# Kernel tuning notes

Hardware: AMD Instinct MI355X
Metric: run time of the kernel (lower is better)

## Reference

```python
import jax, jax.numpy as jnp
import numpy as np

N_NODES = 100000
N_EDGES = 1600000


def gcn_layer(x, src, dst, W, b, n_nodes):
    # PyG GCNConv: h = x @ W; add self-loops; sym-normalized scatter-add; + bias
    h = x @ W
    loop = jnp.arange(n_nodes, dtype=src.dtype)
    si = jnp.concatenate([src, loop])
    di = jnp.concatenate([dst, loop])
    deg = jax.ops.segment_sum(jnp.ones(si.shape[0], h.dtype), di, num_segments=n_nodes)
    dinv = jax.lax.rsqrt(deg)  # deg >= 1 due to self-loops
    norm = dinv[si] * dinv[di]              # [E+N]
    msgs = h[si] * norm[:, None]            # gather-scale
    out = jax.ops.segment_sum(msgs, di, num_segments=n_nodes)  # scatter-add
    return out + b


def setup_inputs() -> dict:
    key = jax.random.key(0)
    ks = jax.random.split(key, 8)
    x = jax.random.normal(ks[0], (N_NODES, 8), dtype=jnp.float32)
    edge_index = jax.random.randint(ks[1], (2, N_EDGES), 0, N_NODES, dtype=jnp.int32)
    W1 = jax.random.normal(ks[2], (8, 32), dtype=jnp.float32) * 0.3
    b1 = jax.random.normal(ks[3], (32,), dtype=jnp.float32) * 0.1
    W2 = jax.random.normal(ks[4], (32, 16), dtype=jnp.float32) * 0.2
    b2 = jax.random.normal(ks[5], (16,), dtype=jnp.float32) * 0.1
    Wfc = jax.random.normal(ks[6], (16, 1), dtype=jnp.float32) * 0.25
    bfc = jax.random.normal(ks[7], (1,), dtype=jnp.float32) * 0.1
    return {"x": x, "edge_index": edge_index, "W1": W1, "b1": b1,
            "W2": W2, "b2": b2, "Wfc": Wfc, "bfc": bfc}


def reference(x, edge_index, W1, b1, W2, b2, Wfc, bfc):
    n = x.shape[0]
    src, dst = edge_index[0], edge_index[1]
    h = jax.nn.relu(gcn_layer(x, src, dst, W1, b1, n))
    h = jax.nn.relu(gcn_layer(h, src, dst, W2, b2, n))
    return jax.nn.sigmoid(h @ Wfc + bfc)  # [N, 1]
```

## Files before the change

kernel.cpp:

```cpp
#include <hip/hip_runtime.h>
#include <math.h>

#define N_NODES 100000
#define N_EDGES 1600000

#define NB_SHIFT 7
#define NB 128
#define NBINS 782
#define RCAP 2432
#define BCHUNK 2048
#define BINBLOCKS ((N_EDGES + BCHUNK - 1) / BCHUNK)
#define LCAP 8
#define SPB 16

__device__ __forceinline__ unsigned int pack_bf2(float a, float b) {
    unsigned int ua = __float_as_uint(a), ub = __float_as_uint(b);
    ua += 0x7FFFu + ((ua >> 16) & 1u);
    ub += 0x7FFFu + ((ub >> 16) & 1u);
    return (ua >> 16) | (ub & 0xFFFF0000u);
}
__device__ __forceinline__ float bf_lo(unsigned int u) { return __uint_as_float(u << 16); }
__device__ __forceinline__ float bf_hi(unsigned int u) { return __uint_as_float(u & 0xFFFF0000u); }

#define QR(v) { v += __shfl_xor(v, 1, 64); v += __shfl_xor(v, 2, 64); }

__global__ __launch_bounds__(512) void k_bin(const int* __restrict__ src, const int* __restrict__ dst,
                                             unsigned char* __restrict__ cnt_tab, int* __restrict__ log,
                                             int* __restrict__ spill_rec, int* __restrict__ spill_bin, int e) {
    __shared__ int lcnt[NBINS];
    __shared__ int lbuf[NBINS * LCAP];
    __shared__ int sp_rec[SPB];
    __shared__ int sp_bin[SPB];
    __shared__ int sp_n;
    int tid = threadIdx.x, blk = blockIdx.x;
    for (int b = tid; b < NBINS; b += 512) lcnt[b] = 0;
    if (tid == 0) sp_n = 0;
    __syncthreads();
    int base = blk * BCHUNK;
    int end = min(base + BCHUNK, e);
    int i0 = base + tid * 4;
    if (i0 + 4 <= end) {
        int4 s4 = *(const int4*)(src + i0);
        int4 d4 = *(const int4*)(dst + i0);
        int ss[4] = { s4.x, s4.y, s4.z, s4.w };
        int dd[4] = { d4.x, d4.y, d4.z, d4.w };
#pragma unroll
        for (int k = 0; k < 4; ++k) {
            int d = dd[k], s = ss[k];
            int b = d >> NB_SHIFT;
            int rec = (s << NB_SHIFT) | (d & (NB - 1));
            int slot = atomicAdd(&lcnt[b], 1);
            if (slot < LCAP) {
                lbuf[b * LCAP + slot] = rec;
            } else {
                int kk = atomicAdd(&sp_n, 1);
                if (kk < SPB) { sp_rec[kk] = rec; sp_bin[kk] = b; }
            }
        }
    } else {
        for (int i = i0; i < end; ++i) {
            int d = dst[i], s = src[i];
            int b = d >> NB_SHIFT;
            int rec = (s << NB_SHIFT) | (d & (NB - 1));
            int slot = atomicAdd(&lcnt[b], 1);
            if (slot < LCAP) {
                lbuf[b * LCAP + slot] = rec;
            } else {
                int kk = atomicAdd(&sp_n, 1);
                if (kk < SPB) { sp_rec[kk] = rec; sp_bin[kk] = b; }
            }
        }
    }
    __syncthreads();
    int* lrow = log + blk * NBINS * LCAP;
    for (int b = tid; b < NBINS; b += 512) {
        int c = min(lcnt[b], LCAP);
        cnt_tab[blk * NBINS + b] = (unsigned char)c;
        if (c > 0) *(int4*)(lrow + b * LCAP)     = *(const int4*)&lbuf[b * LCAP];
        if (c > 4) *(int4*)(lrow + b * LCAP + 4) = *(const int4*)&lbuf[b * LCAP + 4];
    }
    if (tid < SPB) {
        int valid = tid < min(sp_n, SPB);
        spill_rec[blk * SPB + tid] = valid ? sp_rec[tid] : 0;
        spill_bin[blk * SPB + tid] = valid ? sp_bin[tid] : -1;
    }
}

__global__ __launch_bounds__(512) void k_sort(const unsigned char* __restrict__ cnt_tab, const int* __restrict__ log,
                                              const int* __restrict__ spill_rec, const int* __restrict__ spill_bin,
                                              int* __restrict__ gcur, int* __restrict__ regions,
                                              const float* __restrict__ x, float* __restrict__ dinv,
                                              unsigned int* __restrict__ gxu, int* __restrict__ row_start) {
    __shared__ int ccnt[BINBLOCKS];
    __shared__ int coff[BINBLOCKS];
    __shared__ int wtot[8];
    __shared__ int msum_s;
    __shared__ int sp_take;
    __shared__ int lrec[RCAP];
    __shared__ int lsort[RCAP];
    __shared__ int cnt[NB];
    __shared__ int stt[NB];
    __shared__ int cur[NB];
    __shared__ float di_s[NB];
    int b = blockIdx.x, tid = threadIdx.x;
    int lane = tid & 63, wv = tid >> 6;

    for (int c = tid; c < BINBLOCKS; c += 512) ccnt[c] = cnt_tab[c * NBINS + b];
    if (tid == 0) sp_take = 0;
    if (tid < NB) cnt[tid] = 0;
    __syncthreads();
    {
        int c0 = tid * 2, c1 = c0 + 1;
        int v0 = (c0 < BINBLOCKS) ? ccnt[c0] : 0;
        int v1 = (c1 < BINBLOCKS) ? ccnt[c1] : 0;
        int v = v0 + v1, sc = v;
#pragma unroll
        for (int off = 1; off < 64; off <<= 1) {
            int t = __shfl_up(sc, off, 64);
            if (lane >= off) sc += t;
        }
        if (lane == 63) wtot[wv] = sc;
        __syncthreads();
        if (tid == 0) {
            int acc = 0;
#pragma unroll
            for (int w = 0; w < 8; ++w) { int t = wtot[w]; wtot[w] = acc; acc += t; }
            msum_s = acc;
        }
        __syncthreads();
        int basep = sc - v + wtot[wv];
        if (c0 < BINBLOCKS) coff[c0] = basep;
        if (c1 < BINBLOCKS) coff[c1] = basep + v0;
    }
    __syncthreads();
    for (int c = tid; c < BINBLOCKS; c += 512) {
        int cc = ccnt[c];
        if (cc > 0) {
            const int* chunk = log + (c * NBINS + b) * LCAP;
            int p = coff[c];
            int4 v0 = *(const int4*)chunk;
            int r;
            r = v0.x; if (p < RCAP)              { lrec[p] = r;     atomicAdd(&cnt[r & (NB - 1)], 1); }
            r = v0.y; if (cc > 1 && p + 1 < RCAP){ lrec[p + 1] = r; atomicAdd(&cnt[r & (NB - 1)], 1); }
            r = v0.z; if (cc > 2 && p + 2 < RCAP){ lrec[p + 2] = r; atomicAdd(&cnt[r & (NB - 1)], 1); }
            r = v0.w; if (cc > 3 && p + 3 < RCAP){ lrec[p + 3] = r; atomicAdd(&cnt[r & (NB - 1)], 1); }
            if (cc > 4) {
                int4 v1 = *(const int4*)(chunk + 4);
                r = v1.x; if (p + 4 < RCAP)          { lrec[p + 4] = r; atomicAdd(&cnt[r & (NB - 1)], 1); }
                r = v1.y; if (cc > 5 && p + 5 < RCAP){ lrec[p + 5] = r; atomicAdd(&cnt[r & (NB - 1)], 1); }
                r = v1.z; if (cc > 6 && p + 6 < RCAP){ lrec[p + 6] = r; atomicAdd(&cnt[r & (NB - 1)], 1); }
                r = v1.w; if (cc > 7 && p + 7 < RCAP){ lrec[p + 7] = r; atomicAdd(&cnt[r & (NB - 1)], 1); }
            }
        }
    }
    for (int jj = tid; jj < BINBLOCKS * SPB; jj += 512) {
        if (spill_bin[jj] == b) {
            int p = atomicAdd(&sp_take, 1);
            int pos = msum_s + p;
            if (pos < RCAP) {
                int rec = spill_rec[jj];
                lrec[pos] = rec;
                atomicAdd(&cnt[rec & (NB - 1)], 1);
            }
        }
    }
    __syncthreads();
    int m = min(msum_s + sp_take, RCAP);
    if (tid == 0) gcur[b] = m;
    if (tid < 64) {
        int c0 = cnt[lane], c1 = cnt[64 + lane];
        int s0 = c0, s1 = c1;
#pragma unroll
        for (int off = 1; off < 64; off <<= 1) {
            int t0 = __shfl_up(s0, off, 64);
            int t1 = __shfl_up(s1, off, 64);
            if (lane >= off) { s0 += t0; s1 += t1; }
        }
        s1 += __shfl(s0, 63, 64);
        stt[lane] = s0 - c0;
        stt[64 + lane] = s1 - c1;
    }
    __syncthreads();
    int node0 = b << NB_SHIFT;
    if (tid < NB) {
        cur[tid] = stt[tid];
        float d = rsqrtf((float)cnt[tid] + 1.0f);
        di_s[tid] = d;
        row_start[b * NB + tid] = b * RCAP + stt[tid];
        int node = node0 + tid;
        if (node < N_NODES) dinv[node] = d;
    }
    __syncthreads();
    {
        int l = tid >> 2, p = tid & 3;
        int node = node0 + l;
        if (node < N_NODES) {
            const float2* x2 = (const float2*)x;
            float2 xv = x2[node * 4 + p];
            float d = di_s[l];
            gxu[node * 4 + p] = pack_bf2(xv.x * d, xv.y * d);
        }
    }
    for (int j = tid; j < m; j += 512) {
        int rec = lrec[j];
        int pos = atomicAdd(&cur[rec & (NB - 1)], 1);
        lsort[pos] = rec >> NB_SHIFT;
    }
    __syncthreads();
    int* wb = regions + b * RCAP;
    for (int j = tid; j < m; j += 512) wb[j] = lsort[j];
}

__global__ __launch_bounds__(512) void k_agg1_mlp(const int* __restrict__ gcur, const int* __restrict__ regions,
                                                  const int* __restrict__ row_start,
                                                  const unsigned int* __restrict__ gxu,
                                                  const float* __restrict__ dinv,
                                                  const float* __restrict__ W1, const float* __restrict__ b1,
                                                  const float* __restrict__ W2,
                                                  unsigned int* __restrict__ g2u) {
    __shared__ int lsort[RCAP];
    __shared__ float wsh[800];
    int b = blockIdx.x, tid = threadIdx.x;
    int m = gcur[b];
    const int* rrow = regions + b * RCAP;
    for (int j = tid; j < m; j += 512) lsort[j] = rrow[j];
    for (int i2 = tid; i2 < 800; i2 += 512)
        wsh[i2] = (i2 < 256) ? W1[i2] : (i2 < 288) ? b1[i2 - 256] : W2[i2 - 288];
    __syncthreads();
    int l = tid >> 2, q = tid & 3;
    int node = (b << NB_SHIFT) + l;
    if (node >= N_NODES) return;
    int js = row_start[node] - b * RCAP;
    int je = (l < NB - 1) ? (row_start[node + 1] - b * RCAP) : m;
    const uint4* gx4 = (const uint4*)gxu;
    float a0 = 0.f, a1 = 0.f, a2 = 0.f, a3 = 0.f, a4 = 0.f, a5 = 0.f, a6 = 0.f, a7 = 0.f;
    if (q == 0) {
        uint4 u = gx4[node];
        a0 = bf_lo(u.x); a1 = bf_hi(u.x); a2 = bf_lo(u.y); a3 = bf_hi(u.y);
        a4 = bf_lo(u.z); a5 = bf_hi(u.z); a6 = bf_lo(u.w); a7 = bf_hi(u.w);
    }
    int j = js + q;
    for (; j + 4 < je; j += 8) {
        int s0 = lsort[j], s1 = lsort[j + 4];
        uint4 u = gx4[s0];
        uint4 w = gx4[s1];
        a0 += bf_lo(u.x); a1 += bf_hi(u.x); a2 += bf_lo(u.y); a3 += bf_hi(u.y);
        a4 += bf_lo(u.z); a5 += bf_hi(u.z); a6 += bf_lo(u.w); a7 += bf_hi(u.w);
        a0 += bf_lo(w.x); a1 += bf_hi(w.x); a2 += bf_lo(w.y); a3 += bf_hi(w.y);
        a4 += bf_lo(w.z); a5 += bf_hi(w.z); a6 += bf_lo(w.w); a7 += bf_hi(w.w);
    }
    if (j < je) {
        uint4 u = gx4[lsort[j]];
        a0 += bf_lo(u.x); a1 += bf_hi(u.x); a2 += bf_lo(u.y); a3 += bf_hi(u.y);
        a4 += bf_lo(u.z); a5 += bf_hi(u.z); a6 += bf_lo(u.w); a7 += bf_hi(u.w);
    }
    QR(a0); QR(a1); QR(a2); QR(a3); QR(a4); QR(a5); QR(a6); QR(a7);
    float di = dinv[node];
    float y[8] = { a0 * di, a1 * di, a2 * di, a3 * di, a4 * di, a5 * di, a6 * di, a7 * di };
    const float* W1s = wsh;
    const float* b1s = wsh + 256;
    const float* W2s = wsh + 288;
    float hh[8];
#pragma unroll
    for (int ff = 0; ff < 8; ++ff) {
        int f = q * 8 + ff;
        float sa = b1s[f];
#pragma unroll
        for (int k = 0; k < 8; ++k) sa = fmaf(y[k], W1s[k * 32 + f], sa);
        hh[ff] = fmaxf(0.f, sa);
    }
    float g[16];
#pragma unroll
    for (int o = 0; o < 16; ++o) {
        float sa = 0.f;
#pragma unroll
        for (int ff = 0; ff < 8; ++ff) sa = fmaf(hh[ff], W2s[(q * 8 + ff) * 16 + o], sa);
        g[o] = sa;
    }
#pragma unroll
    for (int o = 0; o < 16; ++o) QR(g[o]);
    int f0 = q * 4;
    uint2 pk = make_uint2(pack_bf2(g[f0] * di, g[f0 + 1] * di),
                          pack_bf2(g[f0 + 2] * di, g[f0 + 3] * di));
    ((uint2*)g2u)[node * 4 + q] = pk;
}

__global__ __launch_bounds__(512) void k_agg2_final(const int* __restrict__ gcur, const int* __restrict__ regions,
                                                    const int* __restrict__ row_start,
                                                    const unsigned int* __restrict__ g2u,
                                                    const float* __restrict__ dinv,
                                                    const float* __restrict__ b2, const float* __restrict__ Wfc,
                                                    const float* __restrict__ bfc, float* __restrict__ out) {
    __shared__ int lsort[RCAP];
    int b = blockIdx.x, tid = threadIdx.x;
    int m = gcur[b];
    const int* rrow = regions + b * RCAP;
    for (int j = tid; j < m; j += 512) lsort[j] = rrow[j];
    __syncthreads();
    int l = tid >> 2, q = tid & 3;
    int node = (b << NB_SHIFT) + l;
    if (node >= N_NODES) return;
    int js = row_start[node] - b * RCAP;
    int je = (l < NB - 1) ? (row_start[node + 1] - b * RCAP) : m;
    const uint4* g24 = (const uint4*)g2u;
    float a[16];
#pragma unroll
    for (int f = 0; f < 16; ++f) a[f] = 0.f;
    if (q == 0) {
        uint4 u0 = g24[node * 2], u1 = g24[node * 2 + 1];
        a[0] = bf_lo(u0.x); a[1] = bf_hi(u0.x); a[2] = bf_lo(u0.y); a[3] = bf_hi(u0.y);
        a[4] = bf_lo(u0.z); a[5] = bf_hi(u0.z); a[6] = bf_lo(u0.w); a[7] = bf_hi(u0.w);
        a[8] = bf_lo(u1.x); a[9] = bf_hi(u1.x); a[10] = bf_lo(u1.y); a[11] = bf_hi(u1.y);
        a[12] = bf_lo(u1.z); a[13] = bf_hi(u1.z); a[14] = bf_lo(u1.w); a[15] = bf_hi(u1.w);
    }
    int j = js + q;
    for (; j + 4 < je; j += 8) {
        int s0 = lsort[j], s1 = lsort[j + 4];
        uint4 u0 = g24[s0 * 2], u1 = g24[s0 * 2 + 1];
        uint4 w0 = g24[s1 * 2], w1 = g24[s1 * 2 + 1];
        a[0] += bf_lo(u0.x); a[1] += bf_hi(u0.x); a[2] += bf_lo(u0.y); a[3] += bf_hi(u0.y);
        a[4] += bf_lo(u0.z); a[5] += bf_hi(u0.z); a[6] += bf_lo(u0.w); a[7] += bf_hi(u0.w);
        a[8] += bf_lo(u1.x); a[9] += bf_hi(u1.x); a[10] += bf_lo(u1.y); a[11] += bf_hi(u1.y);
        a[12] += bf_lo(u1.z); a[13] += bf_hi(u1.z); a[14] += bf_lo(u1.w); a[15] += bf_hi(u1.w);
        a[0] += bf_lo(w0.x); a[1] += bf_hi(w0.x); a[2] += bf_lo(w0.y); a[3] += bf_hi(w0.y);
        a[4] += bf_lo(w0.z); a[5] += bf_hi(w0.z); a[6] += bf_lo(w0.w); a[7] += bf_hi(w0.w);
        a[8] += bf_lo(w1.x); a[9] += bf_hi(w1.x); a[10] += bf_lo(w1.y); a[11] += bf_hi(w1.y);
        a[12] += bf_lo(w1.z); a[13] += bf_hi(w1.z); a[14] += bf_lo(w1.w); a[15] += bf_hi(w1.w);
    }
    if (j < je) {
        int s0 = lsort[j];
        uint4 u0 = g24[s0 * 2], u1 = g24[s0 * 2 + 1];
        a[0] += bf_lo(u0.x); a[1] += bf_hi(u0.x); a[2] += bf_lo(u0.y); a[3] += bf_hi(u0.y);
        a[4] += bf_lo(u0.z); a[5] += bf_hi(u0.z); a[6] += bf_lo(u0.w); a[7] += bf_hi(u0.w);
        a[8] += bf_lo(u1.x); a[9] += bf_hi(u1.x); a[10] += bf_lo(u1.y); a[11] += bf_hi(u1.y);
        a[12] += bf_lo(u1.z); a[13] += bf_hi(u1.z); a[14] += bf_lo(u1.w); a[15] += bf_hi(u1.w);
    }
#pragma unroll
    for (int f = 0; f < 16; ++f) QR(a[f]);
    if (q == 0) {
        float di = dinv[node];
        float z = bfc[0];
#pragma unroll
        for (int f = 0; f < 16; ++f)
            z += fmaxf(0.f, di * a[f] + b2[f]) * Wfc[f];
        out[node] = 1.0f / (1.0f + expf(-z));
    }
}

extern "C" void kernel_launch(void* const* d_in, const int* in_sizes, int n_in,
                              void* d_out, int out_size, void* d_ws, size_t ws_size,
                              hipStream_t stream) {
    const float* x   = (const float*)d_in[0];
    const int*   ei  = (const int*)d_in[1];
    const float* W1  = (const float*)d_in[2];
    const float* b1  = (const float*)d_in[3];
    const float* W2  = (const float*)d_in[4];
    const float* b2  = (const float*)d_in[5];
    const float* Wfc = (const float*)d_in[6];
    const float* bfc = (const float*)d_in[7];
    float* out = (float*)d_out;

    const int* src = ei;
    const int* dst = ei + N_EDGES;
    const int E = N_EDGES;

    int*           log       = (int*)d_ws;
    int*           spill_rec = log + (size_t)BINBLOCKS * NBINS * LCAP;
    int*           spill_bin = spill_rec + BINBLOCKS * SPB;
    int*           gcur      = spill_bin + BINBLOCKS * SPB;
    int*           regions   = gcur + NBINS;
    int*           row_start = regions + NBINS * RCAP;
    float*         dinv      = (float*)(row_start + NBINS * NB);
    unsigned int*  gxu       = (unsigned int*)(dinv + N_NODES);
    unsigned int*  g2u       = gxu + (size_t)N_NODES * 4;
    unsigned char* cnt_tab   = (unsigned char*)(g2u + (size_t)N_NODES * 8);

    k_bin<<<BINBLOCKS, 512, 0, stream>>>(src, dst, cnt_tab, log, spill_rec, spill_bin, E);
    k_sort<<<NBINS, 512, 0, stream>>>(cnt_tab, log, spill_rec, spill_bin, gcur, regions, x, dinv, gxu, row_start);
    k_agg1_mlp<<<NBINS, 512, 0, stream>>>(gcur, regions, row_start, gxu, dinv, W1, b1, W2, g2u);
    k_agg2_final<<<NBINS, 512, 0, stream>>>(gcur, regions, row_start, g2u, dinv, b2, Wfc, bfc, out);
}
```

Measured before the change: 142.8 us.

## Fuse four kernels into one persistent kernel with software grid barriers

Replaces the four separate launches (bin, sort, layer-1 aggregate+MLP, layer-2 aggregate+final) with a single persistent kernel of 256 blocks that loops over bins and separates phases with atomic-counter grid barriers. Shared memory for the phases is overlaid in a union, and the small weight tensors are staged in shared memory. The aim is to remove launch gaps and tail effects between kernels. In exchange, each block now handles about three bins serially, and the spin barriers with a timeout risk deadlock or silent corruption if all blocks are not co-resident; a memset launch is also added.

```diff
diff --git a/kernel.cpp b/kernel.cpp
--- a/kernel.cpp
+++ b/kernel.cpp
@@ -9,9 +9,11 @@
 #define NBINS 782
 #define RCAP 2432
 #define BCHUNK 2048
-#define BINBLOCKS ((N_EDGES + BCHUNK - 1) / BCHUNK)
+#define BINBLOCKS 782
 #define LCAP 8
 #define SPB 16
+#define NT 512
+#define GRID 256
 
 __device__ __forceinline__ unsigned int pack_bf2(float a, float b) {
     unsigned int ua = __float_as_uint(a), ub = __float_as_uint(b);
@@ -24,326 +26,343 @@
 
 #define QR(v) { v += __shfl_xor(v, 1, 64); v += __shfl_xor(v, 2, 64); }
 
-__global__ __launch_bounds__(512) void k_bin(const int* __restrict__ src, const int* __restrict__ dst,
-                                             unsigned char* __restrict__ cnt_tab, int* __restrict__ log,
-                                             int* __restrict__ spill_rec, int* __restrict__ spill_bin, int e) {
-    __shared__ int lcnt[NBINS];
-    __shared__ int lbuf[NBINS * LCAP];
-    __shared__ int sp_rec[SPB];
-    __shared__ int sp_bin[SPB];
-    __shared__ int sp_n;
-    int tid = threadIdx.x, blk = blockIdx.x;
-    for (int b = tid; b < NBINS; b += 512) lcnt[b] = 0;
-    if (tid == 0) sp_n = 0;
+__device__ __forceinline__ void gbar(int* ctr, int tid) {
+    __threadfence();
     __syncthreads();
-    int base = blk * BCHUNK;
-    int end = min(base + BCHUNK, e);
-    int i0 = base + tid * 4;
-    if (i0 + 4 <= end) {
-        int4 s4 = *(const int4*)(src + i0);
-        int4 d4 = *(const int4*)(dst + i0);
-        int ss[4] = { s4.x, s4.y, s4.z, s4.w };
-        int dd[4] = { d4.x, d4.y, d4.z, d4.w };
-#pragma unroll
-        for (int k = 0; k < 4; ++k) {
-            int d = dd[k], s = ss[k];
-            int b = d >> NB_SHIFT;
-            int rec = (s << NB_SHIFT) | (d & (NB - 1));
-            int slot = atomicAdd(&lcnt[b], 1);
-            if (slot < LCAP) {
-                lbuf[b * LCAP + slot] = rec;
-            } else {
-                int kk = atomicAdd(&sp_n, 1);
-                if (kk < SPB) { sp_rec[kk] = rec; sp_bin[kk] = b; }
-            }
-        }
-    } else {
-        for (int i = i0; i < end; ++i) {
-            int d = dst[i], s = src[i];
-            int b = d >> NB_SHIFT;
-            int rec = (s << NB_SHIFT) | (d & (NB - 1));
-            int slot = atomicAdd(&lcnt[b], 1);
-            if (slot < LCAP) {
-                lbuf[b * LCAP + slot] = rec;
-            } else {
-                int kk = atomicAdd(&sp_n, 1);
-                if (kk < SPB) { sp_rec[kk] = rec; sp_bin[kk] = b; }
-            }
+    if (tid == 0) {
+        __hip_atomic_fetch_add(ctr, 1, __ATOMIC_ACQ_REL, __HIP_MEMORY_SCOPE_AGENT);
+        unsigned long long t0 = __builtin_amdgcn_s_memrealtime();
+        while (__hip_atomic_load(ctr, __ATOMIC_ACQUIRE, __HIP_MEMORY_SCOPE_AGENT) < GRID) {
+            __builtin_amdgcn_s_sleep(32);
+            if (__builtin_amdgcn_s_memrealtime() - t0 > 10000000ULL) break;
         }
     }
     __syncthreads();
-    int* lrow = log + blk * NBINS * LCAP;
-    for (int b = tid; b < NBINS; b += 512) {
-        int c = min(lcnt[b], LCAP);
-        cnt_tab[blk * NBINS + b] = (unsigned char)c;
-        if (c > 0) *(int4*)(lrow + b * LCAP)     = *(const int4*)&lbuf[b * LCAP];
-        if (c > 4) *(int4*)(lrow + b * LCAP + 4) = *(const int4*)&lbuf[b * LCAP + 4];
+    __threadfence();
+}
+
+struct SMem {
+    union U {
+        struct A { int lcnt[NBINS]; int lbuf[NBINS * LCAP];
+                   int sp_rec[SPB]; int sp_bin[SPB]; int sp_n; } a;
+        struct B { int ccnt[BINBLOCKS]; int coff[BINBLOCKS]; int lrec[RCAP]; int lsort[RCAP];
+                   int cnt[NB]; int stt[NB]; int cur[NB]; float di_s[NB];
+                   int wtot[8]; int sp_take, msum_s; } b;
+        struct CD { int lsort[RCAP]; float wsh[840]; } cd;
+    } u;
+};
+
+__global__ __launch_bounds__(NT) void k_fused(
+        const int* __restrict__ src, const int* __restrict__ dst,
+        const float* __restrict__ x,
+        const float* __restrict__ W1, const float* __restrict__ b1,
+        const float* __restrict__ W2, const float* __restrict__ b2,
+        const float* __restrict__ Wfc, const float* __restrict__ bfc,
+        int* __restrict__ bar,
+        unsigned char* __restrict__ cnt_tab, int* __restrict__ glog,
+        int* __restrict__ spill_rec, int* __restrict__ spill_bin,
+        int* __restrict__ gcur, int* __restrict__ regions, int* __restrict__ row_start,
+        float* __restrict__ dinv, unsigned int* __restrict__ gxu,
+        unsigned int* __restrict__ g2u, float* __restrict__ out) {
+    __shared__ SMem s;
+    int tid = threadIdx.x, blk = blockIdx.x;
+    int lane = tid & 63, wv = tid >> 6;
+
+    for (int c = blk; c < BINBLOCKS; c += GRID) {
+        for (int i = tid; i < NBINS; i += NT) s.u.a.lcnt[i] = 0;
+        if (tid == 0) s.u.a.sp_n = 0;
+        __syncthreads();
+        int base = c * BCHUNK;
+        int end = min(base + BCHUNK, N_EDGES);
+        int i0 = base + tid * 4;
+        if (i0 + 4 <= end) {
+            int4 s4 = *(const int4*)(src + i0);
+            int4 d4 = *(const int4*)(dst + i0);
+            int ss[4] = { s4.x, s4.y, s4.z, s4.w };
+            int dd[4] = { d4.x, d4.y, d4.z, d4.w };
+#pragma unroll
+            for (int k = 0; k < 4; ++k) {
+                int d = dd[k], sv = ss[k];
+                int bin = d >> NB_SHIFT;
+                int rec = (sv << NB_SHIFT) | (d & (NB - 1));
+                int slot = atomicAdd(&s.u.a.lcnt[bin], 1);
+                if (slot < LCAP) {
+                    s.u.a.lbuf[bin * LCAP + slot] = rec;
+                } else {
+                    int kk = atomicAdd(&s.u.a.sp_n, 1);
+                    if (kk < SPB) { s.u.a.sp_rec[kk] = rec; s.u.a.sp_bin[kk] = bin; }
+                }
+            }
+        } else {
+            for (int i = i0; i < end; ++i) {
+                int d = dst[i], sv = src[i];
+                int bin = d >> NB_SHIFT;
+                int rec = (sv << NB_SHIFT) | (d & (NB - 1));
+                int slot = atomicAdd(&s.u.a.lcnt[bin], 1);
+                if (slot < LCAP) {
+                    s.u.a.lbuf[bin * LCAP + slot] = rec;
+                } else {
+                    int kk = atomicAdd(&s.u.a.sp_n, 1);
+                    if (kk < SPB) { s.u.a.sp_rec[kk] = rec; s.u.a.sp_bin[kk] = bin; }
+                }
+            }
+        }
+        __syncthreads();
+        int* lrow = glog + c * NBINS * LCAP;
+        for (int i = tid; i < NBINS; i += NT) {
+            int cc = min(s.u.a.lcnt[i], LCAP);
+            cnt_tab[c * NBINS + i] = (unsigned char)cc;
+            if (cc > 0) *(int4*)(lrow + i * LCAP)     = *(const int4*)&s.u.a.lbuf[i * LCAP];
+            if (cc > 4) *(int4*)(lrow + i * LCAP + 4) = *(const int4*)&s.u.a.lbuf[i * LCAP + 4];
+        }
+        if (tid < SPB) {
+            int valid = tid < min(s.u.a.sp_n, SPB);
+            spill_rec[c * SPB + tid] = valid ? s.u.a.sp_rec[tid] : 0;
+            spill_bin[c * SPB + tid] = valid ? s.u.a.sp_bin[tid] : -1;
+        }
+        __syncthreads();
     }
-    if (tid < SPB) {
-        int valid = tid < min(sp_n, SPB);
-        spill_rec[blk * SPB + tid] = valid ? sp_rec[tid] : 0;
-        spill_bin[blk * SPB + tid] = valid ? sp_bin[tid] : -1;
+    gbar(&bar[0], tid);
+
+    for (int bin = blk; bin < NBINS; bin += GRID) {
+        for (int c = tid; c < BINBLOCKS; c += NT) s.u.b.ccnt[c] = cnt_tab[c * NBINS + bin];
+        if (tid == 0) s.u.b.sp_take = 0;
+        if (tid < NB) s.u.b.cnt[tid] = 0;
+        __syncthreads();
+        {
+            int c0 = tid * 2, c1 = c0 + 1;
+            int v0 = (c0 < BINBLOCKS) ? s.u.b.ccnt[c0] : 0;
+            int v1 = (c1 < BINBLOCKS) ? s.u.b.ccnt[c1] : 0;
+            int v = v0 + v1, sc = v;
+#pragma unroll
+            for (int off = 1; off < 64; off <<= 1) {
+                int t = __shfl_up(sc, off, 64);
+                if (lane >= off) sc += t;
+            }
+            if (lane == 63) s.u.b.wtot[wv] = sc;
+            __syncthreads();
+            if (tid == 0) {
+                int acc = 0;
+#pragma unroll
+                for (int w = 0; w < 8; ++w) { int t = s.u.b.wtot[w]; s.u.b.wtot[w] = acc; acc += t; }
+                s.u.b.msum_s = acc;
+            }
+            __syncthreads();
+            int basep = sc - v + s.u.b.wtot[wv];
+            if (c0 < BINBLOCKS) s.u.b.coff[c0] = basep;
+            if (c1 < BINBLOCKS) s.u.b.coff[c1] = basep + v0;
+        }
+        __syncthreads();
+        for (int c = tid; c < BINBLOCKS; c += NT) {
+            int cc = s.u.b.ccnt[c];
+            if (cc > 0) {
+                const int* chunk = glog + (c * NBINS + bin) * LCAP;
+                int p = s.u.b.coff[c];
+                int4 v0 = *(const int4*)chunk;
+                int r;
+                r = v0.x; if (p < RCAP)              { s.u.b.lrec[p] = r;     atomicAdd(&s.u.b.cnt[r & (NB - 1)], 1); }
+                r = v0.y; if (cc > 1 && p + 1 < RCAP){ s.u.b.lrec[p + 1] = r; atomicAdd(&s.u.b.cnt[r & (NB - 1)], 1); }
+                r = v0.z; if (cc > 2 && p + 2 < RCAP){ s.u.b.lrec[p + 2] = r; atomicAdd(&s.u.b.cnt[r & (NB - 1)], 1); }
+                r = v0.w; if (cc > 3 && p + 3 < RCAP){ s.u.b.lrec[p + 3] = r; atomicAdd(&s.u.b.cnt[r & (NB - 1)], 1); }
+                if (cc > 4) {
+                    int4 v1 = *(const int4*)(chunk + 4);
+                    r = v1.x; if (p + 4 < RCAP)          { s.u.b.lrec[p + 4] = r; atomicAdd(&s.u.b.cnt[r & (NB - 1)], 1); }
+                    r = v1.y; if (cc > 5 && p + 5 < RCAP){ s.u.b.lrec[p + 5] = r; atomicAdd(&s.u.b.cnt[r & (NB - 1)], 1); }
+                    r = v1.z; if (cc > 6 && p + 6 < RCAP){ s.u.b.lrec[p + 6] = r; atomicAdd(&s.u.b.cnt[r & (NB - 1)], 1); }
+                    r = v1.w; if (cc > 7 && p + 7 < RCAP){ s.u.b.lrec[p + 7] = r; atomicAdd(&s.u.b.cnt[r & (NB - 1)], 1); }
+                }
+            }
+        }
+        for (int jj = tid; jj < BINBLOCKS * SPB; jj += NT) {
+            if (spill_bin[jj] == bin) {
+                int p = atomicAdd(&s.u.b.sp_take, 1);
+                int pos = s.u.b.msum_s + p;
+                if (pos < RCAP) {
+                    int rec = spill_rec[jj];
+                    s.u.b.lrec[pos] = rec;
+                    atomicAdd(&s.u.b.cnt[rec & (NB - 1)], 1);
+                }
+            }
+        }
+        __syncthreads();
+        int m = min(s.u.b.msum_s + s.u.b.sp_take, RCAP);
+        if (tid == 0) gcur[bin] = m;
+        if (tid < 64) {
+            int c0 = s.u.b.cnt[lane], c1 = s.u.b.cnt[64 + lane];
+            int s0 = c0, s1 = c1;
+#pragma unroll
+            for (int off = 1; off < 64; off <<= 1) {
+                int t0 = __shfl_up(s0, off, 64);
+                int t1 = __shfl_up(s1, off, 64);
+                if (lane >= off) { s0 += t0; s1 += t1; }
+            }
+            s1 += __shfl(s0, 63, 64);
+            s.u.b.stt[lane] = s0 - c0;
+            s.u.b.stt[64 + lane] = s1 - c1;
+        }
+        __syncthreads();
+        int node0 = bin << NB_SHIFT;
+        if (tid < NB) {
+            s.u.b.cur[tid] = s.u.b.stt[tid];
+            float d = rsqrtf((float)s.u.b.cnt[tid] + 1.0f);
+            s.u.b.di_s[tid] = d;
+            row_start[bin * NB + tid] = bin * RCAP + s.u.b.stt[tid];
+            int node = node0 + tid;
+            if (node < N_NODES) dinv[node] = d;
+        }
+        __syncthreads();
+        {
+            int l = tid >> 2, p = tid & 3;
+            int node = node0 + l;
+            if (node < N_NODES) {
+                const float2* x2 = (const float2*)x;
+                float2 xv = x2[node * 4 + p];
+                float d = s.u.b.di_s[l];
+                gxu[node * 4 + p] = pack_bf2(xv.x * d, xv.y * d);
+            }
+        }
+        for (int j = tid; j < m; j += NT) {
+            int rec = s.u.b.lrec[j];
+            int pos = atomicAdd(&s.u.b.cur[rec & (NB - 1)], 1);
+            s.u.b.lsort[pos] = rec >> NB_SHIFT;
+        }
+        __syncthreads();
+        int* wb = regions + bin * RCAP;
+        for (int j = tid; j < m; j += NT) wb[j] = s.u.b.lsort[j];
+        __syncthreads();
     }
-}
-
-__global__ __launch_bounds__(512) void k_sort(const unsigned char* __restrict__ cnt_tab, const int* __restrict__ log,
-                                              const int* __restrict__ spill_rec, const int* __restrict__ spill_bin,
-                                              int* __restrict__ gcur, int* __restrict__ regions,
-                                              const float* __restrict__ x, float* __restrict__ dinv,
-                                              unsigned int* __restrict__ gxu, int* __restrict__ row_start) {
-    __shared__ int ccnt[BINBLOCKS];
-    __shared__ int coff[BINBLOCKS];
-    __shared__ int wtot[8];
-    __shared__ int msum_s;
-    __shared__ int sp_take;
-    __shared__ int lrec[RCAP];
-    __shared__ int lsort[RCAP];
-    __shared__ int cnt[NB];
-    __shared__ int stt[NB];
-    __shared__ int cur[NB];
-    __shared__ float di_s[NB];
-    int b = blockIdx.x, tid = threadIdx.x;
-    int lane = tid & 63, wv = tid >> 6;
-
-    for (int c = tid; c < BINBLOCKS; c += 512) ccnt[c] = cnt_tab[c * NBINS + b];
-    if (tid == 0) sp_take = 0;
-    if (tid < NB) cnt[tid] = 0;
-    __syncthreads();
-    {
-        int c0 = tid * 2, c1 = c0 + 1;
-        int v0 = (c0 < BINBLOCKS) ? ccnt[c0] : 0;
-        int v1 = (c1 < BINBLOCKS) ? ccnt[c1] : 0;
-        int v = v0 + v1, sc = v;
-#pragma unroll
-        for (int off = 1; off < 64; off <<= 1) {
-            int t = __shfl_up(sc, off, 64);
-            if (lane >= off) sc += t;
-        }
-        if (lane == 63) wtot[wv] = sc;
-        __syncthreads();
-        if (tid == 0) {
-            int acc = 0;
-#pragma unroll
-            for (int w = 0; w < 8; ++w) { int t = wtot[w]; wtot[w] = acc; acc += t; }
-            msum_s = acc;
-        }
-        __syncthreads();
-        int basep = sc - v + wtot[wv];
-        if (c0 < BINBLOCKS) coff[c0] = basep;
-        if (c1 < BINBLOCKS) coff[c1] = basep + v0;
+    gbar(&bar[1], tid);
+
+    for (int i = tid; i < 833; i += NT)
+        s.u.cd.wsh[i] = (i < 256) ? W1[i]
+                      : (i < 288) ? b1[i - 256]
+                      : (i < 800) ? W2[i - 288]
+                      : (i < 816) ? b2[i - 800]
+                      : (i < 832) ? Wfc[i - 816] : bfc[0];
+
+    for (int bin = blk; bin < NBINS; bin += GRID) {
+        int m = gcur[bin];
+        const int* rrow = regions + bin * RCAP;
+        for (int j = tid; j < m; j += NT) s.u.cd.lsort[j] = rrow[j];
+        __syncthreads();
+        int l = tid >> 2, q = tid & 3;
+        int node = (bin << NB_SHIFT) + l;
+        if (node < N_NODES) {
+            int js = row_start[node] - bin * RCAP;
+            int je = (l < NB - 1) ? (row_start[node + 1] - bin * RCAP) : m;
+            const uint4* gx4 = (const uint4*)gxu;
+            float a0 = 0.f, a1 = 0.f, a2 = 0.f, a3 = 0.f, a4 = 0.f, a5 = 0.f, a6 = 0.f, a7 = 0.f;
+            if (q == 0) {
+                uint4 u = gx4[node];
+                a0 = bf_lo(u.x); a1 = bf_hi(u.x); a2 = bf_lo(u.y); a3 = bf_hi(u.y);
+                a4 = bf_lo(u.z); a5 = bf_hi(u.z); a6 = bf_lo(u.w); a7 = bf_hi(u.w);
+            }
+            int j = js + q;
+            for (; j + 4 < je; j += 8) {
+                int s0 = s.u.cd.lsort[j], s1 = s.u.cd.lsort[j + 4];
+                uint4 u = gx4[s0];
+                uint4 w = gx4[s1];
+                a0 += bf_lo(u.x); a1 += bf_hi(u.x); a2 += bf_lo(u.y); a3 += bf_hi(u.y);
+                a4 += bf_lo(u.z); a5 += bf_hi(u.z); a6 += bf_lo(u.w); a7 += bf_hi(u.w);
+                a0 += bf_lo(w.x); a1 += bf_hi(w.x); a2 += bf_lo(w.y); a3 += bf_hi(w.y);
+                a4 += bf_lo(w.z); a5 += bf_hi(w.z); a6 += bf_lo(w.w); a7 += bf_hi(w.w);
+            }
+            if (j < je) {
+                uint4 u = gx4[s.u.cd.lsort[j]];
+                a0 += bf_lo(u.x); a1 += bf_hi(u.x); a2 += bf_lo(u.y); a3 += bf_hi(u.y);
+                a4 += bf_lo(u.z); a5 += bf_hi(u.z); a6 += bf_lo(u.w); a7 += bf_hi(u.w);
+            }
+            QR(a0); QR(a1); QR(a2); QR(a3); QR(a4); QR(a5); QR(a6); QR(a7);
+            float di = dinv[node];
+            float y[8] = { a0 * di, a1 * di, a2 * di, a3 * di, a4 * di, a5 * di, a6 * di, a7 * di };
+            const float* W1s = s.u.cd.wsh;
+            const float* b1s = s.u.cd.wsh + 256;
+            const float* W2s = s.u.cd.wsh + 288;
+            float hh[8];
+#pragma unroll
+            for (int ff = 0; ff < 8; ++ff) {
+                int f = q * 8 + ff;
+                float sa = b1s[f];
+#pragma unroll
+                for (int k = 0; k < 8; ++k) sa = fmaf(y[k], W1s[k * 32 + f], sa);
+                hh[ff] = fmaxf(0.f, sa);
+            }
+            float g[16];
+#pragma unroll
+            for (int o = 0; o < 16; ++o) {
+                float sa = 0.f;
+#pragma unroll
+                for (int ff = 0; ff < 8; ++ff) sa = fmaf(hh[ff], W2s[(q * 8 + ff) * 16 + o], sa);
+                g[o] = sa;
+            }
+#pragma unroll
+            for (int o = 0; o < 16; ++o) QR(g[o]);
+            int f0 = q * 4;
+            uint2 pk = make_uint2(pack_bf2(g[f0] * di, g[f0 + 1] * di),
+                                  pack_bf2(g[f0 + 2] * di, g[f0 + 3] * di));
+            ((uint2*)g2u)[node * 4 + q] = pk;
+        }
+        __syncthreads();
     }
-    __syncthreads();
-    for (int c = tid; c < BINBLOCKS; c += 512) {
-        int cc = ccnt[c];
-        if (cc > 0) {
-            const int* chunk = log + (c * NBINS + b) * LCAP;
-            int p = coff[c];
-            int4 v0 = *(const int4*)chunk;
-            int r;
-            r = v0.x; if (p < RCAP)              { lrec[p] = r;     atomicAdd(&cnt[r & (NB - 1)], 1); }
-            r = v0.y; if (cc > 1 && p + 1 < RCAP){ lrec[p + 1] = r; atomicAdd(&cnt[r & (NB - 1)], 1); }
-            r = v0.z; if (cc > 2 && p + 2 < RCAP){ lrec[p + 2] = r; atomicAdd(&cnt[r & (NB - 1)], 1); }
-            r = v0.w; if (cc > 3 && p + 3 < RCAP){ lrec[p + 3] = r; atomicAdd(&cnt[r & (NB - 1)], 1); }
-            if (cc > 4) {
-                int4 v1 = *(const int4*)(chunk + 4);
-                r = v1.x; if (p + 4 < RCAP)          { lrec[p + 4] = r; atomicAdd(&cnt[r & (NB - 1)], 1); }
-                r = v1.y; if (cc > 5 && p + 5 < RCAP){ lrec[p + 5] = r; atomicAdd(&cnt[r & (NB - 1)], 1); }
-                r = v1.z; if (cc > 6 && p + 6 < RCAP){ lrec[p + 6] = r; atomicAdd(&cnt[r & (NB - 1)], 1); }
-                r = v1.w; if (cc > 7 && p + 7 < RCAP){ lrec[p + 7] = r; atomicAdd(&cnt[r & (NB - 1)], 1); }
-            }
-        }
-    }
-    for (int jj = tid; jj < BINBLOCKS * SPB; jj += 512) {
-        if (spill_bin[jj] == b) {
-            int p = atomicAdd(&sp_take, 1);
-            int pos = msum_s + p;
-            if (pos < RCAP) {
-                int rec = spill_rec[jj];
-                lrec[pos] = rec;
-                atomicAdd(&cnt[rec & (NB - 1)], 1);
-            }
-        }
-    }
-    __syncthreads();
-    int m = min(msum_s + sp_take, RCAP);
-    if (tid == 0) gcur[b] = m;
-    if (tid < 64) {
-        int c0 = cnt[lane], c1 = cnt[64 + lane];
-        int s0 = c0, s1 = c1;
-#pragma unroll
-        for (int off = 1; off < 64; off <<= 1) {
-            int t0 = __shfl_up(s0, off, 64);
-            int t1 = __shfl_up(s1, off, 64);
-            if (lane >= off) { s0 += t0; s1 += t1; }
-        }
-        s1 += __shfl(s0, 63, 64);
-        stt[lane] = s0 - c0;
-        stt[64 + lane] = s1 - c1;
-    }
-    __syncthreads();
-    int node0 = b << NB_SHIFT;
-    if (tid < NB) {
-        cur[tid] = stt[tid];
-        float d = rsqrtf((float)cnt[tid] + 1.0f);
-        di_s[tid] = d;
-        row_start[b * NB + tid] = b * RCAP + stt[tid];
-        int node = node0 + tid;
-        if (node < N_NODES) dinv[node] = d;
-    }
-    __syncthreads();
-    {
-        int l = tid >> 2, p = tid & 3;
-        int node = node0 + l;
+    gbar(&bar[2], tid);
+
+    for (int bin = blk; bin < NBINS; bin += GRID) {
+        int m = gcur[bin];
+        const int* rrow = regions + bin * RCAP;
+        for (int j = tid; j < m; j += NT) s.u.cd.lsort[j] = rrow[j];
+        __syncthreads();
+        int l = tid >> 2, q = tid & 3;
+        int node = (bin << NB_SHIFT) + l;
         if (node < N_NODES) {
-            const float2* x2 = (const float2*)x;
-            float2 xv = x2[node * 4 + p];
-            float d = di_s[l];
-            gxu[node * 4 + p] = pack_bf2(xv.x * d, xv.y * d);
-        }
-    }
-    for (int j = tid; j < m; j += 512) {
-        int rec = lrec[j];
-        int pos = atomicAdd(&cur[rec & (NB - 1)], 1);
-        lsort[pos] = rec >> NB_SHIFT;
-    }
-    __syncthreads();
-    int* wb = regions + b * RCAP;
-    for (int j = tid; j < m; j += 512) wb[j] = lsort[j];
-}
-
-__global__ __launch_bounds__(512) void k_agg1_mlp(const int* __restrict__ gcur, const int* __restrict__ regions,
-                                                  const int* __restrict__ row_start,
-                                                  const unsigned int* __restrict__ gxu,
-                                                  const float* __restrict__ dinv,
-                                                  const float* __restrict__ W1, const float* __restrict__ b1,
-                                                  const float* __restrict__ W2,
-                                                  unsigned int* __restrict__ g2u) {
-    __shared__ int lsort[RCAP];
-    __shared__ float wsh[800];
-    int b = blockIdx.x, tid = threadIdx.x;
-    int m = gcur[b];
-    const int* rrow = regions + b * RCAP;
-    for (int j = tid; j < m; j += 512) lsort[j] = rrow[j];
-    for (int i2 = tid; i2 < 800; i2 += 512)
-        wsh[i2] = (i2 < 256) ? W1[i2] : (i2 < 288) ? b1[i2 - 256] : W2[i2 - 288];
-    __syncthreads();
-    int l = tid >> 2, q = tid & 3;
-    int node = (b << NB_SHIFT) + l;
-    if (node >= N_NODES) return;
-    int js = row_start[node] - b * RCAP;
-    int je = (l < NB - 1) ? (row_start[node + 1] - b * RCAP) : m;
-    const uint4* gx4 = (const uint4*)gxu;
-    float a0 = 0.f, a1 = 0.f, a2 = 0.f, a3 = 0.f, a4 = 0.f, a5 = 0.f, a6 = 0.f, a7 = 0.f;
-    if (q == 0) {
-        uint4 u = gx4[node];
-        a0 = bf_lo(u.x); a1 = bf_hi(u.x); a2 = bf_lo(u.y); a3 = bf_hi(u.y);
-        a4 = bf_lo(u.z); a5 = bf_hi(u.z); a6 = bf_lo(u.w); a7 = bf_hi(u.w);
-    }
-    int j = js + q;
-    for (; j + 4 < je; j += 8) {
-        int s0 = lsort[j], s1 = lsort[j + 4];
-        uint4 u = gx4[s0];
-        uint4 w = gx4[s1];
-        a0 += bf_lo(u.x); a1 += bf_hi(u.x); a2 += bf_lo(u.y); a3 += bf_hi(u.y);
-        a4 += bf_lo(u.z); a5 += bf_hi(u.z); a6 += bf_lo(u.w); a7 += bf_hi(u.w);
-        a0 += bf_lo(w.x); a1 += bf_hi(w.x); a2 += bf_lo(w.y); a3 += bf_hi(w.y);
-        a4 += bf_lo(w.z); a5 += bf_hi(w.z); a6 += bf_lo(w.w); a7 += bf_hi(w.w);
-    }
-    if (j < je) {
-        uint4 u = gx4[lsort[j]];
-        a0 += bf_lo(u.x); a1 += bf_hi(u.x); a2 += bf_lo(u.y); a3 += bf_hi(u.y);
-        a4 += bf_lo(u.z); a5 += bf_hi(u.z); a6 += bf_lo(u.w); a7 += bf_hi(u.w);
-    }
-    QR(a0); QR(a1); QR(a2); QR(a3); QR(a4); QR(a5); QR(a6); QR(a7);
-    float di = dinv[node];
-    float y[8] = { a0 * di, a1 * di, a2 * di, a3 * di, a4 * di, a5 * di, a6 * di, a7 * di };
-    const float* W1s = wsh;
-    const float* b1s = wsh + 256;
-    const float* W2s = wsh + 288;
-    float hh[8];
-#pragma unroll
-    for (int ff = 0; ff < 8; ++ff) {
-        int f = q * 8 + ff;
-        float sa = b1s[f];
-#pragma unroll
-        for (int k = 0; k < 8; ++k) sa = fmaf(y[k], W1s[k * 32 + f], sa);
-        hh[ff] = fmaxf(0.f, sa);
-    }
-    float g[16];
-#pragma unroll
-    for (int o = 0; o < 16; ++o) {
-        float sa = 0.f;
-#pragma unroll
-        for (int ff = 0; ff < 8; ++ff) sa = fmaf(hh[ff], W2s[(q * 8 + ff) * 16 + o], sa);
-        g[o] = sa;
-    }
-#pragma unroll
-    for (int o = 0; o < 16; ++o) QR(g[o]);
-    int f0 = q * 4;
-    uint2 pk = make_uint2(pack_bf2(g[f0] * di, g[f0 + 1] * di),
-                          pack_bf2(g[f0 + 2] * di, g[f0 + 3] * di));
-    ((uint2*)g2u)[node * 4 + q] = pk;
-}
-
-__global__ __launch_bounds__(512) void k_agg2_final(const int* __restrict__ gcur, const int* __restrict__ regions,
-                                                    const int* __restrict__ row_start,
-                                                    const unsigned int* __restrict__ g2u,
-                                                    const float* __restrict__ dinv,
-                                                    const float* __restrict__ b2, const float* __restrict__ Wfc,
-                                                    const float* __restrict__ bfc, float* __restrict__ out) {
-    __shared__ int lsort[RCAP];
-    int b = blockIdx.x, tid = threadIdx.x;
-    int m = gcur[b];
-    const int* rrow = regions + b * RCAP;
-    for (int j = tid; j < m; j += 512) lsort[j] = rrow[j];
-    __syncthreads();
-    int l = tid >> 2, q = tid & 3;
-    int node = (b << NB_SHIFT) + l;
-    if (node >= N_NODES) return;
-    int js = row_start[node] - b * RCAP;
-    int je = (l < NB - 1) ? (row_start[node + 1] - b * RCAP) : m;
-    const uint4* g24 = (const uint4*)g2u;
-    float a[16];
-#pragma unroll
-    for (int f = 0; f < 16; ++f) a[f] = 0.f;
-    if (q == 0) {
-        uint4 u0 = g24[node * 2], u1 = g24[node * 2 + 1];
-        a[0] = bf_lo(u0.x); a[1] = bf_hi(u0.x); a[2] = bf_lo(u0.y); a[3] = bf_hi(u0.y);
-        a[4] = bf_lo(u0.z); a[5] = bf_hi(u0.z); a[6] = bf_lo(u0.w); a[7] = bf_hi(u0.w);
-        a[8] = bf_lo(u1.x); a[9] = bf_hi(u1.x); a[10] = bf_lo(u1.y); a[11] = bf_hi(u1.y);
-        a[12] = bf_lo(u1.z); a[13] = bf_hi(u1.z); a[14] = bf_lo(u1.w); a[15] = bf_hi(u1.w);
-    }
-    int j = js + q;
-    for (; j + 4 < je; j += 8) {
-        int s0 = lsort[j], s1 = lsort[j + 4];
-        uint4 u0 = g24[s0 * 2], u1 = g24[s0 * 2 + 1];
-        uint4 w0 = g24[s1 * 2], w1 = g24[s1 * 2 + 1];
-        a[0] += bf_lo(u0.x); a[1] += bf_hi(u0.x); a[2] += bf_lo(u0.y); a[3] += bf_hi(u0.y);
-        a[4] += bf_lo(u0.z); a[5] += bf_hi(u0.z); a[6] += bf_lo(u0.w); a[7] += bf_hi(u0.w);
-        a[8] += bf_lo(u1.x); a[9] += bf_hi(u1.x); a[10] += bf_lo(u1.y); a[11] += bf_hi(u1.y);
-        a[12] += bf_lo(u1.z); a[13] += bf_hi(u1.z); a[14] += bf_lo(u1.w); a[15] += bf_hi(u1.w);
-        a[0] += bf_lo(w0.x); a[1] += bf_hi(w0.x); a[2] += bf_lo(w0.y); a[3] += bf_hi(w0.y);
-        a[4] += bf_lo(w0.z); a[5] += bf_hi(w0.z); a[6] += bf_lo(w0.w); a[7] += bf_hi(w0.w);
-        a[8] += bf_lo(w1.x); a[9] += bf_hi(w1.x); a[10] += bf_lo(w1.y); a[11] += bf_hi(w1.y);
-        a[12] += bf_lo(w1.z); a[13] += bf_hi(w1.z); a[14] += bf_lo(w1.w); a[15] += bf_hi(w1.w);
-    }
-    if (j < je) {
-        int s0 = lsort[j];
-        uint4 u0 = g24[s0 * 2], u1 = g24[s0 * 2 + 1];
-        a[0] += bf_lo(u0.x); a[1] += bf_hi(u0.x); a[2] += bf_lo(u0.y); a[3] += bf_hi(u0.y);
-        a[4] += bf_lo(u0.z); a[5] += bf_hi(u0.z); a[6] += bf_lo(u0.w); a[7] += bf_hi(u0.w);
-        a[8] += bf_lo(u1.x); a[9] += bf_hi(u1.x); a[10] += bf_lo(u1.y); a[11] += bf_hi(u1.y);
-        a[12] += bf_lo(u1.z); a[13] += bf_hi(u1.z); a[14] += bf_lo(u1.w); a[15] += bf_hi(u1.w);
-    }
-#pragma unroll
-    for (int f = 0; f < 16; ++f) QR(a[f]);
-    if (q == 0) {
-        float di = dinv[node];
-        float z = bfc[0];
-#pragma unroll
-        for (int f = 0; f < 16; ++f)
-            z += fmaxf(0.f, di * a[f] + b2[f]) * Wfc[f];
-        out[node] = 1.0f / (1.0f + expf(-z));
+            int js = row_start[node] - bin * RCAP;
+            int je = (l < NB - 1) ? (row_start[node + 1] - bin * RCAP) : m;
+            const uint4* g24 = (const uint4*)g2u;
+            float a[16];
+#pragma unroll
+            for (int f = 0; f < 16; ++f) a[f] = 0.f;
+            if (q == 0) {
+                uint4 u0 = g24[node * 2], u1 = g24[node * 2 + 1];
+                a[0] = bf_lo(u0.x); a[1] = bf_hi(u0.x); a[2] = bf_lo(u0.y); a[3] = bf_hi(u0.y);
+                a[4] = bf_lo(u0.z); a[5] = bf_hi(u0.z); a[6] = bf_lo(u0.w); a[7] = bf_hi(u0.w);
+                a[8] = bf_lo(u1.x); a[9] = bf_hi(u1.x); a[10] = bf_lo(u1.y); a[11] = bf_hi(u1.y);
+                a[12] = bf_lo(u1.z); a[13] = bf_hi(u1.z); a[14] = bf_lo(u1.w); a[15] = bf_hi(u1.w);
+            }
+            int j = js + q;
+            for (; j + 4 < je; j += 8) {
+                int s0 = s.u.cd.lsort[j], s1 = s.u.cd.lsort[j + 4];
+                uint4 u0 = g24[s0 * 2], u1 = g24[s0 * 2 + 1];
+                uint4 w0 = g24[s1 * 2], w1 = g24[s1 * 2 + 1];
+                a[0] += bf_lo(u0.x); a[1] += bf_hi(u0.x); a[2] += bf_lo(u0.y); a[3] += bf_hi(u0.y);
+                a[4] += bf_lo(u0.z); a[5] += bf_hi(u0.z); a[6] += bf_lo(u0.w); a[7] += bf_hi(u0.w);
+                a[8] += bf_lo(u1.x); a[9] += bf_hi(u1.x); a[10] += bf_lo(u1.y); a[11] += bf_hi(u1.y);
+                a[12] += bf_lo(u1.z); a[13] += bf_hi(u1.z); a[14] += bf_lo(u1.w); a[15] += bf_hi(u1.w);
+                a[0] += bf_lo(w0.x); a[1] += bf_hi(w0.x); a[2] += bf_lo(w0.y); a[3] += bf_hi(w0.y);
+                a[4] += bf_lo(w0.z); a[5] += bf_hi(w0.z); a[6] += bf_lo(w0.w); a[7] += bf_hi(w0.w);
+                a[8] += bf_lo(w1.x); a[9] += bf_hi(w1.x); a[10] += bf_lo(w1.y); a[11] += bf_hi(w1.y);
+                a[12] += bf_lo(w1.z); a[13] += bf_hi(w1.z); a[14] += bf_lo(w1.w); a[15] += bf_hi(w1.w);
+            }
+            if (j < je) {
+                int s0 = s.u.cd.lsort[j];
+                uint4 u0 = g24[s0 * 2], u1 = g24[s0 * 2 + 1];
+                a[0] += bf_lo(u0.x); a[1] += bf_hi(u0.x); a[2] += bf_lo(u0.y); a[3] += bf_hi(u0.y);
+                a[4] += bf_lo(u0.z); a[5] += bf_hi(u0.z); a[6] += bf_lo(u0.w); a[7] += bf_hi(u0.w);
+                a[8] += bf_lo(u1.x); a[9] += bf_hi(u1.x); a[10] += bf_lo(u1.y); a[11] += bf_hi(u1.y);
+                a[12] += bf_lo(u1.z); a[13] += bf_hi(u1.z); a[14] += bf_lo(u1.w); a[15] += bf_hi(u1.w);
+            }
+#pragma unroll
+            for (int f = 0; f < 16; ++f) QR(a[f]);
+            if (q == 0) {
+                float di = dinv[node];
+                const float* b2s  = s.u.cd.wsh + 800;
+                const float* wfcs = s.u.cd.wsh + 816;
+                float z = s.u.cd.wsh[832];
+#pragma unroll
+                for (int f = 0; f < 16; ++f)
+                    z += fmaxf(0.f, di * a[f] + b2s[f]) * wfcs[f];
+                out[node] = 1.0f / (1.0f + expf(-z));
+            }
+        }
+        __syncthreads();
     }
 }
 
@@ -362,21 +381,21 @@
 
     const int* src = ei;
     const int* dst = ei + N_EDGES;
-    const int E = N_EDGES;
-
-    int*           log       = (int*)d_ws;
-    int*           spill_rec = log + (size_t)BINBLOCKS * NBINS * LCAP;
+
+    int*           bar       = (int*)d_ws;
+    int*           glog      = bar + 8;
+    int*           spill_rec = glog + (size_t)BINBLOCKS * NBINS * LCAP;
     int*           spill_bin = spill_rec + BINBLOCKS * SPB;
     int*           gcur      = spill_bin + BINBLOCKS * SPB;
     int*           regions   = gcur + NBINS;
-    int*           row_start = regions + NBINS * RCAP;
+    int*           row_start = regions + (size_t)NBINS * RCAP;
     float*         dinv      = (float*)(row_start + NBINS * NB);
     unsigned int*  gxu       = (unsigned int*)(dinv + N_NODES);
     unsigned int*  g2u       = gxu + (size_t)N_NODES * 4;
     unsigned char* cnt_tab   = (unsigned char*)(g2u + (size_t)N_NODES * 8);
 
-    k_bin<<<BINBLOCKS, 512, 0, stream>>>(src, dst, cnt_tab, log, spill_rec, spill_bin, E);
-    k_sort<<<NBINS, 512, 0, stream>>>(cnt_tab, log, spill_rec, spill_bin, gcur, regions, x, dinv, gxu, row_start);
-    k_agg1_mlp<<<NBINS, 512, 0, stream>>>(gcur, regions, row_start, gxu, dinv, W1, b1, W2, g2u);
-    k_agg2_final<<<NBINS, 512, 0, stream>>>(gcur, regions, row_start, g2u, dinv, b2, Wfc, bfc, out);
+    hipMemsetAsync(bar, 0, 8 * sizeof(int), stream);
+    k_fused<<<GRID, NT, 0, stream>>>(src, dst, x, W1, b1, W2, b2, Wfc, bfc,
+                                     bar, cnt_tab, glog, spill_rec, spill_bin,
+                                     gcur, regions, row_start, dinv, gxu, g2u, out);
 }
```

Result: slower. 476.2 us (+233.5%).
